# Kernel optimization log

Hardware: AMD Instinct MI355X
Metric: run time of the kernel (lower is better)

## Reference

```python
import jax, jax.numpy as jnp
import numpy as np

B, S, H = 4, 2048, 1024
NH, HD, G = 16, 64, 8          # heads, head_dim, groups
GD = HD // G                   # group_dim = 8
SCALE_MIN, SCALE_MAX = 0.9, 1.1


def setup_inputs() -> dict:
    key = jax.random.key(0)
    ks = jax.random.split(key, 9)
    std = 1.0 / np.sqrt(H)
    return {
        "hidden_states": jax.random.normal(ks[0], (B, S, H), jnp.float32),
        "Wq": jax.random.normal(ks[1], (H, H), jnp.float32) * std,
        "bq": jax.random.normal(ks[2], (H,), jnp.float32) * std,
        "Wk": jax.random.normal(ks[3], (H, H), jnp.float32) * std,
        "bk": jax.random.normal(ks[4], (H,), jnp.float32) * std,
        "Wv": jax.random.normal(ks[5], (H, H), jnp.float32) * std,
        "bv": jax.random.normal(ks[6], (H,), jnp.float32) * std,
        "Ws": jax.random.normal(ks[7], (H, NH * G), jnp.float32) * std,
        "bs": jax.random.normal(ks[8], (NH * G,), jnp.float32) * std,
    }


def _shape_heads(x):
    # [B,S,H] -> [B,h,S,D]
    return x.reshape(B, S, NH, HD).transpose(0, 2, 1, 3)


def reference(hidden_states, Wq, bq, Wk, bk, Wv, bv, Ws, bs):
    Q = _shape_heads(hidden_states @ Wq + bq)
    K = _shape_heads(hidden_states @ Wk + bk)
    V = _shape_heads(hidden_states @ Wv + bv)

    # per-(head, group) dynamic scale in [scale_min, scale_max]
    s_logits = hidden_states @ Ws + bs                     # [B,S,h*g]
    s = jax.nn.sigmoid(s_logits) * (SCALE_MAX - SCALE_MIN) + SCALE_MIN
    s = s.reshape(B, S, NH, G).transpose(0, 2, 1, 3)       # [B,h,S,g]
    s = jnp.repeat(s, GD, axis=-1)                          # [B,h,S,D]

    Q = Q * s  # apply_to == 'q'

    attn_scores = jnp.einsum('bhsd,bhtd->bhst', Q, K) / np.sqrt(HD).astype(np.float32)
    attn_probs = jax.nn.softmax(attn_scores, axis=-1)
    context = jnp.einsum('bhst,bhtd->bhsd', attn_probs, V)
    context = context.transpose(0, 2, 1, 3).reshape(B, S, NH * HD)
    return context
```

## Files before the change

kernel.cpp:

```cpp
#include <hip/hip_runtime.h>
#include <hip/hip_bf16.h>
#include <stdint.h>

typedef short bf16x8 __attribute__((ext_vector_type(8)));
typedef float f32x4 __attribute__((ext_vector_type(4)));
typedef unsigned short u16;
typedef unsigned short u16x4 __attribute__((ext_vector_type(4)));
typedef unsigned short u16x8 __attribute__((ext_vector_type(8)));

#define LOG2E 1.44269504088896f

#define Bz 4
#define Sz 2048
#define Hz 1024
#define NHz 16
#define HDz 64

__device__ __forceinline__ u16 f2bf(float f) {
  uint32_t u = __builtin_bit_cast(uint32_t, f);
  u += 0x7fffu + ((u >> 16) & 1u);
  return (u16)(u >> 16);
}
__device__ __forceinline__ float bf2f(u16 h) {
  uint32_t u = ((uint32_t)h) << 16;
  return __builtin_bit_cast(float, u);
}
__device__ __forceinline__ u16 f2bfrn(float f) {
  return __builtin_bit_cast(u16, __float2bfloat16(f));
}

__device__ __forceinline__ void gll16(const void* g, void* l) {
  __builtin_amdgcn_global_load_lds((const __attribute__((address_space(1))) void*)g,
                                   (__attribute__((address_space(3))) void*)l,
                                   16, 0, 0);
}

__global__ void k_cvt_x(const float* __restrict__ X, u16* __restrict__ Xb) {
  int i = blockIdx.x * 256 + threadIdx.x;
  float4 v = ((const float4*)X)[i];
  u16x4 r;
  r[0] = f2bf(v.x); r[1] = f2bf(v.y); r[2] = f2bf(v.z); r[3] = f2bf(v.w);
  ((u16x4*)Xb)[i] = r;
}

__global__ void k_cvt_w(const float* __restrict__ Wq, const float* __restrict__ Wk,
                        const float* __restrict__ Wv, const float* __restrict__ Ws,
                        u16* __restrict__ Wt) {
  __shared__ float tile[64][65];
  int n0 = blockIdx.x * 64, k0 = blockIdx.y * 64;
  const float* src; int ld, c0;
  if (n0 < 1024)      { src = Wq; ld = 1024; c0 = n0; }
  else if (n0 < 2048) { src = Wk; ld = 1024; c0 = n0 - 1024; }
  else if (n0 < 3072) { src = Wv; ld = 1024; c0 = n0 - 2048; }
  else                { src = Ws; ld = 128;  c0 = n0 - 3072; }
  int t = threadIdx.x;
  #pragma unroll
  for (int i = 0; i < 16; ++i) {
    int idx = t + i * 256; int r = idx >> 6, c = idx & 63;
    tile[r][c] = src[(size_t)(k0 + r) * ld + c0 + c];
  }
  __syncthreads();
  #pragma unroll
  for (int i = 0; i < 16; ++i) {
    int idx = t + i * 256; int rn = idx >> 6, ck = idx & 63;
    Wt[(size_t)(n0 + rn) * 1024 + k0 + ck] = f2bf(tile[ck][rn]);
  }
}

__launch_bounds__(512, 6)
__global__ void k_gemm(const u16* __restrict__ Xb, const u16* __restrict__ Wt,
                       const float* __restrict__ bq, const float* __restrict__ bk,
                       const float* __restrict__ bv, const float* __restrict__ bs,
                       u16* __restrict__ Qw, u16* __restrict__ Kw, u16* __restrict__ Vw,
                       float* __restrict__ Sw) {
  __shared__ u16 As[128 * 64];
  __shared__ u16 Bs[128 * 64];
  int t = threadIdx.x, lane = t & 63;
  int l15 = lane & 15, g = lane >> 4;
  int wave = t >> 6, wr = wave >> 2, wc = wave & 3;

  int p = blockIdx.x;
  int xcd = p & 7;
  int idx = p >> 3;
  int n_t = idx >> 3;
  int m_t = xcd * 8 + (idx & 7);
  int m0 = m_t * 128, n0 = n_t * 128;

  f32x4 acc[4][2];
  #pragma unroll
  for (int i = 0; i < 4; ++i)
    #pragma unroll
    for (int j = 0; j < 2; ++j) { f32x4 z = {0.f,0.f,0.f,0.f}; acc[i][j] = z; }

  int srow = t >> 3;
  int sob  = (t & 7) << 4;

  const char* Ag = (const char*)Xb;
  const char* Bg = (const char*)Wt;

  {
    int row = srow;
    int sb = sob ^ ((row & 7) << 4);
    gll16(Ag + (size_t)(m0 + row) * 2048 + sb, (char*)As + row * 128 + sob);
    gll16(Bg + (size_t)(n0 + row) * 2048 + sb, (char*)Bs + row * 128 + sob);
    row = 64 + srow;
    sb = sob ^ ((row & 7) << 4);
    gll16(Ag + (size_t)(m0 + row) * 2048 + sb, (char*)As + row * 128 + sob);
    gll16(Bg + (size_t)(n0 + row) * 2048 + sb, (char*)Bs + row * 128 + sob);
  }
  __syncthreads();

  for (int kt = 0; kt < 16; ++kt) {
    #pragma unroll
    for (int ksub = 0; ksub < 2; ++ksub) {
      bf16x8 af[4], bfr[2];
      #pragma unroll
      for (int ai = 0; ai < 4; ++ai) {
        int row = wr * 64 + ai * 16 + l15;
        af[ai] = *(const bf16x8*)((const char*)As + row * 128 +
                                  ((ksub * 64 + 16 * g) ^ ((row & 7) << 4)));
      }
      #pragma unroll
      for (int bj = 0; bj < 2; ++bj) {
        int row = wc * 32 + bj * 16 + l15;
        bfr[bj] = *(const bf16x8*)((const char*)Bs + row * 128 +
                                   ((ksub * 64 + 16 * g) ^ ((row & 7) << 4)));
      }
      #pragma unroll
      for (int ai = 0; ai < 4; ++ai)
        #pragma unroll
        for (int bj = 0; bj < 2; ++bj)
          acc[ai][bj] = __builtin_amdgcn_mfma_f32_16x16x32_bf16(af[ai], bfr[bj], acc[ai][bj], 0, 0, 0);
    }
    if (kt + 1 < 16) {
      __syncthreads();
      size_t kb = (size_t)(kt + 1) * 128;
      int row = srow;
      int sb = sob ^ ((row & 7) << 4);
      gll16(Ag + (size_t)(m0 + row) * 2048 + kb + sb, (char*)As + row * 128 + sob);
      gll16(Bg + (size_t)(n0 + row) * 2048 + kb + sb, (char*)Bs + row * 128 + sob);
      row = 64 + srow;
      sb = sob ^ ((row & 7) << 4);
      gll16(Ag + (size_t)(m0 + row) * 2048 + kb + sb, (char*)As + row * 128 + sob);
      gll16(Bg + (size_t)(n0 + row) * 2048 + kb + sb, (char*)Bs + row * 128 + sob);
      __syncthreads();
    }
  }

  #pragma unroll
  for (int ai = 0; ai < 4; ++ai) {
    #pragma unroll
    for (int bj = 0; bj < 2; ++bj) {
      #pragma unroll
      for (int r = 0; r < 4; ++r) {
        int m = m0 + wr * 64 + ai * 16 + ((lane >> 4) << 2) + r;
        int j = n0 + wc * 32 + bj * 16 + l15;
        float v = acc[ai][bj][r];
        int b = m >> 11, si = m & 2047;
        if (j < 3072) {
          float bias = (j < 1024) ? bq[j] : (j < 2048) ? bk[j - 1024] : bv[j - 2048];
          v += bias;
          int jj = j & 1023, h = jj >> 6, d = jj & 63;
          size_t dst = (((size_t)(b * NHz + h) * Sz + si) << 6) + d;
          u16 hv = f2bf(v);
          if (j < 1024) Qw[dst] = hv;
          else if (j < 2048) Kw[dst] = hv;
          else Vw[dst] = hv;
        } else {
          int c = j - 3072;
          v += bs[c];
          float sig = 1.0f / (1.0f + __expf(-v));
          Sw[(size_t)m * 128 + c] = (0.9f + 0.2f * sig) * 0.125f * LOG2E;
        }
      }
    }
  }
}

__global__ void k_scale_q(u16* __restrict__ Qw, const float* __restrict__ Sw) {
  int tid = blockIdx.x * 256 + threadIdx.x;
  size_t base = (size_t)tid * 8;
  int bh = (int)(base >> 17);
  int si = (int)((base >> 6) & 2047);
  int d0 = (int)(base & 63);
  int b = bh >> 4, h = bh & 15;
  float s = Sw[((size_t)(b * Sz + si)) * 128 + h * 8 + (d0 >> 3)];
  u16x8 v = *(u16x8*)(Qw + base);
  #pragma unroll
  for (int j = 0; j < 8; ++j) v[j] = f2bf(bf2f(v[j]) * s);
  *(u16x8*)(Qw + base) = v;
}

__global__ void k_trans_v(const u16* __restrict__ Vw, u16* __restrict__ Vt) {
  __shared__ u16 tile[64][65];
  int bh = blockIdx.y, s0 = blockIdx.x * 64;
  int t = threadIdx.x;
  const u16* src = Vw + ((size_t)bh * Sz + s0) * 64;
  #pragma unroll
  for (int i = 0; i < 16; ++i) {
    int idx = t + i * 256; int r = idx >> 6, c = idx & 63;
    tile[r][c] = src[r * 64 + c];
  }
  __syncthreads();
  u16* dst = Vt + (size_t)bh * 64 * Sz;
  #pragma unroll
  for (int i = 0; i < 16; ++i) {
    int idx = t + i * 256; int d = idx >> 6, ss = idx & 63;
    dst[(size_t)d * Sz + s0 + ss] = tile[ss][d];
  }
}

__launch_bounds__(256)
__global__ void k_attn(const u16* __restrict__ Qw, const u16* __restrict__ Kw,
                       const u16* __restrict__ Vt, const float* __restrict__ Swp,
                       float* __restrict__ out) {
  __shared__ u16 Kl[2][64 * 64];
  __shared__ u16 Vl[2][64 * 64];
  __shared__ u16 Pl[4][16 * 64];

  int t = threadIdx.x, lane = t & 63, wave = t >> 6;
  int l15 = lane & 15, g = lane >> 4;
  int bh = blockIdx.x, b = bh >> 4, h = bh & 15;
  int q0 = blockIdx.y * 128 + wave * 32;

  const u16* Qb = Qw + (size_t)bh * Sz * 64;
  const char* Kg = (const char*)(Kw + (size_t)bh * Sz * 64);
  const char* Vg = (const char*)(Vt + (size_t)bh * 64 * Sz);
  u16* Pw = Pl[wave];
  int swp = (l15 & 7) << 4;

  int srow = t >> 3;
  int sobyte = (t & 7) << 4;

  bf16x8 qf[2][2];
  #pragma unroll
  for (int qi = 0; qi < 2; ++qi)
    #pragma unroll
    for (int ks = 0; ks < 2; ++ks)
      qf[qi][ks] = *(const bf16x8*)(Qb + (size_t)(q0 + 16 * qi + l15) * 64 + 32 * ks + 8 * g);
  if (Swp) {
    #pragma unroll
    for (int qi = 0; qi < 2; ++qi) {
      size_t m = (size_t)(b * Sz + q0 + 16 * qi + l15);
      #pragma unroll
      for (int ks = 0; ks < 2; ++ks) {
        float s = Swp[m * 128 + h * 8 + 4 * ks + g];
        bf16x8 q = qf[qi][ks];
        #pragma unroll
        for (int j = 0; j < 8; ++j) q[j] = (short)f2bf(bf2f((u16)q[j]) * s);
        qf[qi][ks] = q;
      }
    }
  }

  bf16x8 ones;
  #pragma unroll
  for (int j = 0; j < 8; ++j) ones[j] = (short)0x3F80;

  f32x4 o[2][4], lacc[2];
  #pragma unroll
  for (int qi = 0; qi < 2; ++qi) {
    f32x4 z = {0.f,0.f,0.f,0.f};
    lacc[qi] = z;
    #pragma unroll
    for (int nt = 0; nt < 4; ++nt) o[qi][nt] = z;
  }

  #pragma unroll
  for (int c = 0; c < 2; ++c) {
    int row = c * 32 + srow;
    int sw2 = (row & 7) << 4;
    gll16(Kg + (size_t)row * 128 + (sobyte ^ sw2), (char*)Kl[0] + row * 128 + sobyte);
    gll16(Vg + (size_t)row * (Sz * 2) + (sobyte ^ sw2), (char*)Vl[0] + row * 128 + sobyte);
  }
  __syncthreads();

  int cur = 0;
  for (int kv0 = 0; kv0 < Sz; kv0 += 64) {
    if (kv0 + 64 < Sz) {
      int nxt = cur ^ 1, kvn = kv0 + 64;
      #pragma unroll
      for (int c = 0; c < 2; ++c) {
        int row = c * 32 + srow;
        int sw2 = (row & 7) << 4;
        gll16(Kg + (size_t)(kvn + row) * 128 + (sobyte ^ sw2),
              (char*)Kl[nxt] + row * 128 + sobyte);
        gll16(Vg + (size_t)row * (Sz * 2) + (size_t)kvn * 2 + (sobyte ^ sw2),
              (char*)Vl[nxt] + row * 128 + sobyte);
      }
    }
    const char* Kb = (const char*)Kl[cur];
    const char* Vb = (const char*)Vl[cur];

    f32x4 sc[2][4];
    __builtin_amdgcn_s_setprio(1);
    #pragma unroll
    for (int nt = 0; nt < 4; ++nt) {
      int row = 16 * nt + l15;
      int sw2 = (row & 7) << 4;
      bf16x8 kf0 = *(const bf16x8*)(Kb + row * 128 + ((16 * g) ^ sw2));
      bf16x8 kf1 = *(const bf16x8*)(Kb + row * 128 + ((64 + 16 * g) ^ sw2));
      #pragma unroll
      for (int qi = 0; qi < 2; ++qi) {
        f32x4 a = {0.f,0.f,0.f,0.f};
        a = __builtin_amdgcn_mfma_f32_16x16x32_bf16(kf0, qf[qi][0], a, 0, 0, 0);
        a = __builtin_amdgcn_mfma_f32_16x16x32_bf16(kf1, qf[qi][1], a, 0, 0, 0);
        sc[qi][nt] = a;
      }
    }
    __builtin_amdgcn_s_setprio(0);

    bf16x8 pa[2][2];
    #pragma unroll
    for (int qi = 0; qi < 2; ++qi) {
      int rbase = l15 * 128;
      #pragma unroll
      for (int nt = 0; nt < 4; ++nt) {
        float p0 = __builtin_amdgcn_exp2f(sc[qi][nt][0]);
        float p1 = __builtin_amdgcn_exp2f(sc[qi][nt][1]);
        float p2 = __builtin_amdgcn_exp2f(sc[qi][nt][2]);
        float p3 = __builtin_amdgcn_exp2f(sc[qi][nt][3]);
        u16x4 pk;
        pk[0] = f2bfrn(p0); pk[1] = f2bfrn(p1);
        pk[2] = f2bfrn(p2); pk[3] = f2bfrn(p3);
        *(u16x4*)((char*)Pw + rbase + ((32 * nt + 8 * g) ^ swp)) = pk;
      }
      #pragma unroll
      for (int ks = 0; ks < 2; ++ks)
        pa[qi][ks] = *(const bf16x8*)((char*)Pw + rbase + ((64 * ks + 16 * g) ^ swp));
    }

    __builtin_amdgcn_s_setprio(1);
    #pragma unroll
    for (int ks = 0; ks < 2; ++ks) {
      #pragma unroll
      for (int qi = 0; qi < 2; ++qi)
        lacc[qi] = __builtin_amdgcn_mfma_f32_16x16x32_bf16(pa[qi][ks], ones, lacc[qi], 0, 0, 0);
      #pragma unroll
      for (int nt = 0; nt < 4; ++nt) {
        int row = 16 * nt + l15;
        int sw2 = (row & 7) << 4;
        bf16x8 vf = *(const bf16x8*)(Vb + row * 128 + ((64 * ks + 16 * g) ^ sw2));
        o[0][nt] = __builtin_amdgcn_mfma_f32_16x16x32_bf16(pa[0][ks], vf, o[0][nt], 0, 0, 0);
        o[1][nt] = __builtin_amdgcn_mfma_f32_16x16x32_bf16(pa[1][ks], vf, o[1][nt], 0, 0, 0);
      }
    }
    __builtin_amdgcn_s_setprio(0);
    __syncthreads();
    cur ^= 1;
  }

  #pragma unroll
  for (int qi = 0; qi < 2; ++qi) {
    #pragma unroll
    for (int r = 0; r < 4; ++r) {
      float inv = 1.0f / lacc[qi][r];
      #pragma unroll
      for (int nt = 0; nt < 4; ++nt)
        out[((size_t)(b * Sz + q0 + 16 * qi + 4 * g + r)) * (NHz * HDz) +
            h * 64 + 16 * nt + l15] = o[qi][nt][r] * inv;
    }
  }
}

extern "C" void kernel_launch(void* const* d_in, const int* in_sizes, int n_in,
                              void* d_out, int out_size, void* d_ws, size_t ws_size,
                              hipStream_t stream) {
  const float* X  = (const float*)d_in[0];
  const float* Wq = (const float*)d_in[1];
  const float* bq = (const float*)d_in[2];
  const float* Wk = (const float*)d_in[3];
  const float* bk = (const float*)d_in[4];
  const float* Wv = (const float*)d_in[5];
  const float* bv = (const float*)d_in[6];
  const float* Ws = (const float*)d_in[7];
  const float* bs = (const float*)d_in[8];
  float* out = (float*)d_out;

  char* ws = (char*)d_ws;
  u16* Qw = (u16*)(ws);
  u16* Kw = (u16*)(ws + (size_t)(16u << 20));
  u16* Vw = (u16*)(ws + (size_t)(32u << 20));
  u16* Vt = (u16*)(ws + (size_t)(48u << 20));

  char* ob = (char*)d_out;
  u16* Xb   = (u16*)ob;
  u16* Wt   = (u16*)(ob + (size_t)(16u << 20));

  bool fused = ws_size >= ((size_t)(64u << 20) + (size_t)(4u << 20));
  float* Sw = fused ? (float*)(ws + (size_t)(64u << 20))
                    : (float*)(ob + (size_t)(24u << 20));

  k_cvt_x<<<8192, 256, 0, stream>>>(X, Xb);
  k_cvt_w<<<dim3(50, 16), 256, 0, stream>>>(Wq, Wk, Wv, Ws, Wt);
  k_gemm<<<1600, 512, 0, stream>>>(Xb, Wt, bq, bk, bv, bs, Qw, Kw, Vw, Sw);
  if (!fused) k_scale_q<<<4096, 256, 0, stream>>>(Qw, Sw);
  k_trans_v<<<dim3(32, 64), 256, 0, stream>>>(Vw, Vt);
  k_attn<<<dim3(64, 16), 256, 0, stream>>>(Qw, Kw, Vt, fused ? Sw : nullptr, out);
}
```

Measured before the change: 198.8 us.

## Load K/V fragments directly from global into registers, drop LDS staging

```diff
diff --git a/kernel.cpp b/kernel.cpp
--- a/kernel.cpp
+++ b/kernel.cpp
@@ -210,12 +210,10 @@
   }
 }
 
-__launch_bounds__(256)
+__launch_bounds__(256, 2)
 __global__ void k_attn(const u16* __restrict__ Qw, const u16* __restrict__ Kw,
                        const u16* __restrict__ Vt, const float* __restrict__ Swp,
                        float* __restrict__ out) {
-  __shared__ u16 Kl[2][64 * 64];
-  __shared__ u16 Vl[2][64 * 64];
   __shared__ u16 Pl[4][16 * 64];
 
   int t = threadIdx.x, lane = t & 63, wave = t >> 6;
@@ -224,13 +222,10 @@
   int q0 = blockIdx.y * 128 + wave * 32;
 
   const u16* Qb = Qw + (size_t)bh * Sz * 64;
-  const char* Kg = (const char*)(Kw + (size_t)bh * Sz * 64);
-  const char* Vg = (const char*)(Vt + (size_t)bh * 64 * Sz);
+  const u16* Kb = Kw + (size_t)bh * Sz * 64;
+  const u16* Vb = Vt + (size_t)bh * 64 * Sz;
   u16* Pw = Pl[wave];
   int swp = (l15 & 7) << 4;
-
-  int srow = t >> 3;
-  int sobyte = (t & 7) << 4;
 
   bf16x8 qf[2][2];
   #pragma unroll
@@ -266,45 +261,33 @@
     for (int nt = 0; nt < 4; ++nt) o[qi][nt] = z;
   }
 
-  #pragma unroll
-  for (int c = 0; c < 2; ++c) {
-    int row = c * 32 + srow;
-    int sw2 = (row & 7) << 4;
-    gll16(Kg + (size_t)row * 128 + (sobyte ^ sw2), (char*)Kl[0] + row * 128 + sobyte);
-    gll16(Vg + (size_t)row * (Sz * 2) + (sobyte ^ sw2), (char*)Vl[0] + row * 128 + sobyte);
-  }
-  __syncthreads();
-
-  int cur = 0;
-  for (int kv0 = 0; kv0 < Sz; kv0 += 64) {
-    if (kv0 + 64 < Sz) {
-      int nxt = cur ^ 1, kvn = kv0 + 64;
-      #pragma unroll
-      for (int c = 0; c < 2; ++c) {
-        int row = c * 32 + srow;
-        int sw2 = (row & 7) << 4;
-        gll16(Kg + (size_t)(kvn + row) * 128 + (sobyte ^ sw2),
-              (char*)Kl[nxt] + row * 128 + sobyte);
-        gll16(Vg + (size_t)row * (Sz * 2) + (size_t)kvn * 2 + (sobyte ^ sw2),
-              (char*)Vl[nxt] + row * 128 + sobyte);
-      }
-    }
-    const char* Kb = (const char*)Kl[cur];
-    const char* Vb = (const char*)Vl[cur];
-
+  auto loadK = [&](int kv0, bf16x8 (&kf)[4][2]) {
+    #pragma unroll
+    for (int nt = 0; nt < 4; ++nt) {
+      const u16* p = Kb + (size_t)(kv0 + 16 * nt + l15) * 64 + 8 * g;
+      kf[nt][0] = *(const bf16x8*)p;
+      kf[nt][1] = *(const bf16x8*)(p + 32);
+    }
+  };
+  auto loadV = [&](int kv0, bf16x8 (&vf)[2][4]) {
+    #pragma unroll
+    for (int ks = 0; ks < 2; ++ks)
+      #pragma unroll
+      for (int nt = 0; nt < 4; ++nt)
+        vf[ks][nt] = *(const bf16x8*)(Vb + (size_t)(16 * nt + l15) * Sz +
+                                      kv0 + 32 * ks + 8 * g);
+  };
+
+  auto tile = [&](const bf16x8 (&kf)[4][2], const bf16x8 (&vf)[2][4]) {
     f32x4 sc[2][4];
     __builtin_amdgcn_s_setprio(1);
     #pragma unroll
     for (int nt = 0; nt < 4; ++nt) {
-      int row = 16 * nt + l15;
-      int sw2 = (row & 7) << 4;
-      bf16x8 kf0 = *(const bf16x8*)(Kb + row * 128 + ((16 * g) ^ sw2));
-      bf16x8 kf1 = *(const bf16x8*)(Kb + row * 128 + ((64 + 16 * g) ^ sw2));
       #pragma unroll
       for (int qi = 0; qi < 2; ++qi) {
         f32x4 a = {0.f,0.f,0.f,0.f};
-        a = __builtin_amdgcn_mfma_f32_16x16x32_bf16(kf0, qf[qi][0], a, 0, 0, 0);
-        a = __builtin_amdgcn_mfma_f32_16x16x32_bf16(kf1, qf[qi][1], a, 0, 0, 0);
+        a = __builtin_amdgcn_mfma_f32_16x16x32_bf16(kf[nt][0], qf[qi][0], a, 0, 0, 0);
+        a = __builtin_amdgcn_mfma_f32_16x16x32_bf16(kf[nt][1], qf[qi][1], a, 0, 0, 0);
         sc[qi][nt] = a;
       }
     }
@@ -338,17 +321,29 @@
         lacc[qi] = __builtin_amdgcn_mfma_f32_16x16x32_bf16(pa[qi][ks], ones, lacc[qi], 0, 0, 0);
       #pragma unroll
       for (int nt = 0; nt < 4; ++nt) {
-        int row = 16 * nt + l15;
-        int sw2 = (row & 7) << 4;
-        bf16x8 vf = *(const bf16x8*)(Vb + row * 128 + ((64 * ks + 16 * g) ^ sw2));
-        o[0][nt] = __builtin_amdgcn_mfma_f32_16x16x32_bf16(pa[0][ks], vf, o[0][nt], 0, 0, 0);
-        o[1][nt] = __builtin_amdgcn_mfma_f32_16x16x32_bf16(pa[1][ks], vf, o[1][nt], 0, 0, 0);
+        o[0][nt] = __builtin_amdgcn_mfma_f32_16x16x32_bf16(pa[0][ks], vf[ks][nt], o[0][nt], 0, 0, 0);
+        o[1][nt] = __builtin_amdgcn_mfma_f32_16x16x32_bf16(pa[1][ks], vf[ks][nt], o[1][nt], 0, 0, 0);
       }
     }
     __builtin_amdgcn_s_setprio(0);
-    __syncthreads();
-    cur ^= 1;
-  }
+  };
+
+  bf16x8 kf[4][2], vf[2][4];
+  loadK(0, kf);
+  loadV(0, vf);
+  for (int tt = 0; tt < 31; ++tt) {
+    bf16x8 kfn[4][2], vfn[2][4];
+    loadK((tt + 1) * 64, kfn);
+    loadV((tt + 1) * 64, vfn);
+    tile(kf, vf);
+    #pragma unroll
+    for (int nt = 0; nt < 4; ++nt) { kf[nt][0] = kfn[nt][0]; kf[nt][1] = kfn[nt][1]; }
+    #pragma unroll
+    for (int ks = 0; ks < 2; ++ks)
+      #pragma unroll
+      for (int nt = 0; nt < 4; ++nt) vf[ks][nt] = vfn[ks][nt];
+  }
+  tile(kf, vf);
 
   #pragma unroll
   for (int qi = 0; qi < 2; ++qi) {
```

After: 330.5 us. 1.66x slower.

## Single-buffer K/V tiles in attention to raise occupancy

Applied to the files above, without the earlier changes.

```diff
diff --git a/kernel.cpp b/kernel.cpp
--- a/kernel.cpp
+++ b/kernel.cpp
@@ -210,12 +210,12 @@
   }
 }
 
-__launch_bounds__(256)
+__launch_bounds__(256, 6)
 __global__ void k_attn(const u16* __restrict__ Qw, const u16* __restrict__ Kw,
                        const u16* __restrict__ Vt, const float* __restrict__ Swp,
                        float* __restrict__ out) {
-  __shared__ u16 Kl[2][64 * 64];
-  __shared__ u16 Vl[2][64 * 64];
+  __shared__ u16 Kl[64 * 64];
+  __shared__ u16 Vl[64 * 64];
   __shared__ u16 Pl[4][16 * 64];
 
   int t = threadIdx.x, lane = t & 63, wave = t >> 6;
@@ -266,40 +266,30 @@
     for (int nt = 0; nt < 4; ++nt) o[qi][nt] = z;
   }
 
-  #pragma unroll
-  for (int c = 0; c < 2; ++c) {
-    int row = c * 32 + srow;
-    int sw2 = (row & 7) << 4;
-    gll16(Kg + (size_t)row * 128 + (sobyte ^ sw2), (char*)Kl[0] + row * 128 + sobyte);
-    gll16(Vg + (size_t)row * (Sz * 2) + (sobyte ^ sw2), (char*)Vl[0] + row * 128 + sobyte);
-  }
+  auto stage = [&](int kv0) {
+    #pragma unroll
+    for (int c = 0; c < 2; ++c) {
+      int row = c * 32 + srow;
+      int sw2 = (row & 7) << 4;
+      gll16(Kg + (size_t)(kv0 + row) * 128 + (sobyte ^ sw2),
+            (char*)Kl + row * 128 + sobyte);
+      gll16(Vg + (size_t)row * (Sz * 2) + (size_t)kv0 * 2 + (sobyte ^ sw2),
+            (char*)Vl + row * 128 + sobyte);
+    }
+  };
+
+  stage(0);
   __syncthreads();
 
-  int cur = 0;
   for (int kv0 = 0; kv0 < Sz; kv0 += 64) {
-    if (kv0 + 64 < Sz) {
-      int nxt = cur ^ 1, kvn = kv0 + 64;
-      #pragma unroll
-      for (int c = 0; c < 2; ++c) {
-        int row = c * 32 + srow;
-        int sw2 = (row & 7) << 4;
-        gll16(Kg + (size_t)(kvn + row) * 128 + (sobyte ^ sw2),
-              (char*)Kl[nxt] + row * 128 + sobyte);
-        gll16(Vg + (size_t)row * (Sz * 2) + (size_t)kvn * 2 + (sobyte ^ sw2),
-              (char*)Vl[nxt] + row * 128 + sobyte);
-      }
-    }
-    const char* Kb = (const char*)Kl[cur];
-    const char* Vb = (const char*)Vl[cur];
-
     f32x4 sc[2][4];
     __builtin_amdgcn_s_setprio(1);
     #pragma unroll
     for (int nt = 0; nt < 4; ++nt) {
       int row = 16 * nt + l15;
       int sw2 = (row & 7) << 4;
-      bf16x8 kf0 = *(const bf16x8*)(Kb + row * 128 + ((16 * g) ^ sw2));
-      bf16x8 kf1 = *(const bf16x8*)(Kb + row * 128 + ((64 + 16 * g) ^ sw2));
+      bf16x8 kf0 = *(const bf16x8*)((const char*)Kl + row * 128 + ((16 * g) ^ sw2));
+      bf16x8 kf1 = *(const bf16x8*)((const char*)Kl + row * 128 + ((64 + 16 * g) ^ sw2));
       #pragma unroll
       for (int qi = 0; qi < 2; ++qi) {
         f32x4 a = {0.f,0.f,0.f,0.f};
@@ -340,14 +330,18 @@
       for (int nt = 0; nt < 4; ++nt) {
         int row = 16 * nt + l15;
         int sw2 = (row & 7) << 4;
-        bf16x8 vf = *(const bf16x8*)(Vb + row * 128 + ((64 * ks + 16 * g) ^ sw2));
+        bf16x8 vf = *(const bf16x8*)((const char*)Vl + row * 128 + ((64 * ks + 16 * g) ^ sw2));
         o[0][nt] = __builtin_amdgcn_mfma_f32_16x16x32_bf16(pa[0][ks], vf, o[0][nt], 0, 0, 0);
         o[1][nt] = __builtin_amdgcn_mfma_f32_16x16x32_bf16(pa[1][ks], vf, o[1][nt], 0, 0, 0);
       }
     }
     __builtin_amdgcn_s_setprio(0);
-    __syncthreads();
-    cur ^= 1;
+
+    if (kv0 + 64 < Sz) {
+      __syncthreads();
+      stage(kv0 + 64);
+      __syncthreads();
+    }
   }
 
   #pragma unroll
```

Measured after the change: 506.3 us. +154.8%, slower.
